# Optimization experiments

Measured on AMD Instinct MI355X. Metric: run time of the kernel, lower is better.

The kernel has to match this reference:

```python
import jax, jax.numpy as jnp
import numpy as np

N_NODES = 50000
N_EDGES = 400000
N_GRAPHS = 512
F = 32        # num_features
NB = 32       # mp_num_basis_fn
ZMAX = 118
CUTOFF = 5.0
NSPH = 9      # (mp_max_degree+1)^2 with max_degree=2
DEG_IDX = jnp.array([0, 1, 1, 1, 2, 2, 2, 2, 2])  # degree of each spherical component


def _bernstein(u, n=NB):
    # reciprocal_bernstein radial basis: Bernstein polynomials of degree n-1 at u in [0,1)
    k = jnp.arange(n, dtype=jnp.float32)
    log_binom = (jax.scipy.special.gammaln(float(n)) - jax.scipy.special.gammaln(k + 1.0)
                 - jax.scipy.special.gammaln(float(n) - k))
    u = jnp.clip(u, 1e-7, 1.0 - 1e-7)[..., None]
    return jnp.exp(log_binom + k * jnp.log(u) + (float(n) - 1.0 - k) * jnp.log1p(-u))


def _smooth_cutoff(r, cutoff=CUTOFF):
    t = r / cutoff
    return jnp.where(t < 1.0, jnp.exp(1.0 - 1.0 / jnp.clip(1.0 - t * t, 1e-7, None)), 0.0)


def _sph(u):
    # real spherical harmonics (cartesian normalization) up to degree 2; u: (E,3) unit vectors
    x, y, z = u[:, 0], u[:, 1], u[:, 2]
    c = jnp.sqrt(jnp.float32(3.0))
    return jnp.stack([jnp.ones_like(x), y, z, x,
                      c * x * y, c * y * z, 0.5 * (3.0 * z * z - 1.0),
                      c * z * x, 0.5 * c * (x * x - y * y)], axis=-1)


def _dense(x, W, b):
    # equivariant Dense: shared kernel over spherical components, bias only on scalar (l=0)
    y = jnp.einsum('nmf,fg->nmg', x, W)
    return y.at[:, 0, :].add(b)


def _silu_gate(x):
    # equivariant silu: scalar channel gates all degrees (scalar part -> exact silu)
    return x * jax.nn.sigmoid(x[:, 0:1, :])


def setup_inputs() -> dict:
    key = jax.random.key(0)
    ks = jax.random.split(key, 24)
    s = 1.0 / np.sqrt(F)
    sb = 1.0 / np.sqrt(NB)
    inp = {
        'positions': 2.0 * jax.random.normal(ks[0], (N_NODES, 3), jnp.float32),
        'embed': jax.random.normal(ks[1], (ZMAX, F), jnp.float32),
        'Wy0': sb * jax.random.normal(ks[2], (3, NB, F), jnp.float32),
        'Wx0': sb * jax.random.normal(ks[3], (3, NB, F), jnp.float32),
        'W1_0': s * jax.random.normal(ks[4], (F, F), jnp.float32),
        'b1_0': jnp.zeros((F,), jnp.float32),
        'W2_0': s * jax.random.normal(ks[5], (F, F), jnp.float32),
        'b2_0': jnp.zeros((F,), jnp.float32),
        'c0': jnp.full((1,), 0.5, jnp.float32),
        'Wr_last': sb * jax.random.normal(ks[6], (NB, F), jnp.float32),
        'W1_1': s * jax.random.normal(ks[7], (F, F), jnp.float32),
        'b1_1': jnp.zeros((F,), jnp.float32),
        'W2_1': s * jax.random.normal(ks[8], (F, F), jnp.float32),
        'b2_1': jnp.zeros((F,), jnp.float32),
        'c1': jnp.full((1,), 0.5, jnp.float32),
        'Wro1': s * jax.random.normal(ks[9], (F, F), jnp.float32),
        'bro1': jnp.zeros((F,), jnp.float32),
        'Wro2': s * jax.random.normal(ks[10], (F, 1), jnp.float32),
        'bro2': jnp.zeros((1,), jnp.float32),
        'atomic_bias': jax.random.normal(ks[11], (ZMAX,), jnp.float32),
        'atomic_numbers': jax.random.randint(ks[12], (N_NODES,), 0, ZMAX, jnp.int32),
        'dst_idx': jax.random.randint(ks[13], (N_EDGES,), 0, N_NODES, jnp.int32),
        'src_idx': jax.random.randint(ks[14], (N_EDGES,), 0, N_NODES, jnp.int32),
        'batch_segments': jnp.sort(jax.random.randint(ks[15], (N_NODES,), 0, N_GRAPHS, jnp.int32)),
        'graph_mask': jnp.ones((N_GRAPHS,), jnp.bool_),
    }
    return inp


def reference(positions, embed, Wy0, Wx0, W1_0, b1_0, W2_0, b2_0, c0,
              Wr_last, W1_1, b1_1, W2_1, b2_1, c1,
              Wro1, bro1, Wro2, bro2, atomic_bias,
              atomic_numbers, dst_idx, src_idx, batch_segments, graph_mask):
    # --- edge geometry (gather_src/gather_dst) ---
    disp = positions[src_idx] - positions[dst_idx]                # (E,3)
    r = jnp.sqrt(jnp.sum(disp * disp, axis=-1) + 1e-12)           # (E,)
    u = disp / r[:, None]
    Y = _sph(u)                                                   # (E,9)
    rbf = _bernstein(r / (r + 1.0)) * _smooth_cutoff(r)[:, None]  # (E,NB)

    # --- atomic embedding, lifted to (N, 9, F) with zero higher degrees ---
    x0 = embed[atomic_numbers]                                    # (N,F)
    x = jnp.concatenate([x0[:, None, :], jnp.zeros((N_NODES, NSPH - 1, F), x0.dtype)], axis=1)

    # --- iteration 0: full-degree equivariant message pass ---
    wy = jnp.einsum('eb,lbf->elf', rbf, Wy0)[:, DEG_IDX, :]       # (E,9,F) radial weights, (0,l)->l path
    wx = jnp.einsum('eb,lbf->elf', rbf, Wx0)[:, DEG_IDX, :]       # (l,0)->l path
    xs = x[src_idx]                                               # (E,9,F)
    msg = wy * Y[:, :, None] * xs[:, 0:1, :] + wx * xs
    y = jax.ops.segment_sum(msg, dst_idx, num_segments=N_NODES)   # (N,9,F)
    y = x + y
    y = _silu_gate(_dense(y, W1_0, b1_0))
    y = _dense(y, W2_0, b2_0)
    x = x + jax.nn.silu(c0) * y                                   # y_nl == 0 (era disabled)

    # --- iteration 1 (last): max_degree=0 message pass, then reduce to scalars ---
    w0 = rbf @ Wr_last                                            # (E,F)
    msg0 = w0 * x[src_idx, 0, :]
    y0 = jax.ops.segment_sum(msg0, dst_idx, num_segments=N_NODES) # (N,F)
    xs0 = x[:, 0, :]                                              # change_max_degree -> scalars
    y0 = xs0 + y0
    y0 = jax.nn.silu(y0 @ W1_1 + b1_1)
    y0 = y0 @ W2_1 + b2_1
    xs0 = xs0 + jax.nn.silu(c1) * y0

    # --- atomic readout and per-graph sum ---
    h = jax.nn.silu(xs0 @ Wro1 + bro1)
    e_atom = (h @ Wro2)[:, 0] + bro2[0] + atomic_bias[atomic_numbers]
    e_graph = jax.ops.segment_sum(e_atom, batch_segments, num_segments=N_GRAPHS)
    return jnp.where(graph_mask, e_graph, 0.0)
```

## Files before the change

### kernel.cpp

```cpp
#include <hip/hip_runtime.h>
#include <math.h>

#define NNODES 50000
#define NEDGES 400000
#define NGRAPHS 512
#define FDIM 32
#define CAP 32

#define NHALVES 4096
#define NQ   (NNODES / NHALVES)
#define NREM (NNODES % NHALVES)

static constexpr float BINOM31[32] = {
    1.f, 31.f, 465.f, 4495.f, 31465.f, 169911.f, 736281.f, 2629575.f,
    7888725.f, 20160075.f, 44352165.f, 84672315.f, 141120525.f, 206253075.f,
    265182525.f, 300540195.f, 300540195.f, 265182525.f, 206253075.f,
    141120525.f, 84672315.f, 44352165.f, 20160075.f, 7888725.f, 2629575.f,
    736281.f, 169911.f, 31465.f, 4495.f, 465.f, 31.f, 1.f
};

__device__ __forceinline__ float fast_rcp(float x) {
    return __builtin_amdgcn_rcpf(x);
}
__device__ __forceinline__ float silu(float x) {
    return x * fast_rcp(1.0f + __expf(-x));
}

__global__ __launch_bounds__(256) void build_csr(
    const float* __restrict__ pos,
    const int* __restrict__ srci, const int* __restrict__ dsti,
    const int* __restrict__ Z,
    float4* __restrict__ pay, int* __restrict__ deg)
{
    int e = blockIdx.x * 256 + threadIdx.x;
    if (e >= NEDGES) return;
    int s = srci[e], d = dsti[e];
    float dx = pos[3 * s]     - pos[3 * d];
    float dy = pos[3 * s + 1] - pos[3 * d + 1];
    float dz = pos[3 * s + 2] - pos[3 * d + 2];
    float r = sqrtf(dx * dx + dy * dy + dz * dz + 1e-12f);
    if (r >= 5.0f) return;

    float t = r * 0.2f;
    float q = fmaxf(1.0f - t * t, 1e-7f);
    float cut = __expf(1.0f - fast_rcp(q));
    float v = fast_rcp(r + 1.0f);
    float v2 = v * v, v4 = v2 * v2, v8 = v4 * v4, v16 = v8 * v8;
    float scale = v16 * v8 * v4 * v2 * v * cut;

    int rank = atomicAdd(&deg[d], 1);
    if (rank < CAP)
        pay[(size_t)d * CAP + rank] =
            make_float4(r, scale,
                        __int_as_float(s * FDIM),
                        __int_as_float(Z[s] * FDIM));
}

#define GATHER8(ACC, XSRC, SEL)                                            \
    float ACC = 0.0f;                                                      \
    for (int j = 0; j < dgc; j += 8) {                                     \
        float rr[8], sc[8], xg[8], hh[8];                                  \
        _Pragma("unroll")                                                  \
        for (int k = 0; k < 8; ++k) {                                      \
            float4 _p = pl[j + k];                                         \
            rr[k] = _p.x; sc[k] = _p.y;                                    \
            xg[k] = (XSRC)[__float_as_int(_p.SEL) + f];                    \
        }                                                                  \
        _Pragma("unroll")                                                  \
        for (int k = 0; k < 8; ++k) hh[k] = cw[31];                        \
        _Pragma("unroll")                                                  \
        for (int t = 30; t >= 0; --t) {                                    \
            _Pragma("unroll")                                              \
            for (int k = 0; k < 8; ++k)                                    \
                hh[k] = fmaf(hh[k], rr[k], cw[t]);                         \
        }                                                                  \
        _Pragma("unroll")                                                  \
        for (int k = 0; k < 8; ++k)                                        \
            ACC = fmaf(sc[k] * hh[k], xg[k], ACC);                         \
    }

#define MATVEC32R(RES, WR, BIAS) do {                                      \
    float4 _q0=yp[0], _q1=yp[1], _q2=yp[2], _q3=yp[3];                     \
    float4 _q4=yp[4], _q5=yp[5], _q6=yp[6], _q7=yp[7];                     \
    float _a0=(BIAS), _a1=0.f, _a2=0.f, _a3=0.f;                           \
    _a0=fmaf(_q0.x,WR[ 0],_a0); _a0=fmaf(_q0.y,WR[ 1],_a0);                \
    _a0=fmaf(_q0.z,WR[ 2],_a0); _a0=fmaf(_q0.w,WR[ 3],_a0);                \
    _a1=fmaf(_q1.x,WR[ 4],_a1); _a1=fmaf(_q1.y,WR[ 5],_a1);                \
    _a1=fmaf(_q1.z,WR[ 6],_a1); _a1=fmaf(_q1.w,WR[ 7],_a1);                \
    _a2=fmaf(_q2.x,WR[ 8],_a2); _a2=fmaf(_q2.y,WR[ 9],_a2);                \
    _a2=fmaf(_q2.z,WR[10],_a2); _a2=fmaf(_q2.w,WR[11],_a2);                \
    _a3=fmaf(_q3.x,WR[12],_a3); _a3=fmaf(_q3.y,WR[13],_a3);                \
    _a3=fmaf(_q3.z,WR[14],_a3); _a3=fmaf(_q3.w,WR[15],_a3);                \
    _a0=fmaf(_q4.x,WR[16],_a0); _a0=fmaf(_q4.y,WR[17],_a0);                \
    _a0=fmaf(_q4.z,WR[18],_a0); _a0=fmaf(_q4.w,WR[19],_a0);                \
    _a1=fmaf(_q5.x,WR[20],_a1); _a1=fmaf(_q5.y,WR[21],_a1);                \
    _a1=fmaf(_q5.z,WR[22],_a1); _a1=fmaf(_q5.w,WR[23],_a1);                \
    _a2=fmaf(_q6.x,WR[24],_a2); _a2=fmaf(_q6.y,WR[25],_a2);                \
    _a2=fmaf(_q6.z,WR[26],_a2); _a2=fmaf(_q6.w,WR[27],_a2);                \
    _a3=fmaf(_q7.x,WR[28],_a3); _a3=fmaf(_q7.y,WR[29],_a3);                \
    _a3=fmaf(_q7.z,WR[30],_a3); _a3=fmaf(_q7.w,WR[31],_a3);                \
    RES = (_a0+_a1)+(_a2+_a3); } while (0)

__device__ __forceinline__ void half_range(int h, int& n0, int& n1) {
    int a = h < NREM ? h * (NQ + 1) : NREM * (NQ + 1) + (h - NREM) * NQ;
    n0 = a;
    n1 = a + (h < NREM ? NQ + 1 : NQ);
}

__global__ __launch_bounds__(256, 2) void fused_a(
    const float4* __restrict__ pay, const int* __restrict__ deg,
    const float* __restrict__ embed, const int* __restrict__ Z,
    const float* __restrict__ Wy0, const float* __restrict__ Wx0,
    const float* __restrict__ W1, const float* __restrict__ b1,
    const float* __restrict__ W2, const float* __restrict__ b2,
    const float* __restrict__ c0,
    float* __restrict__ x1buf)
{
    __shared__ __align__(16) float ylds[4][64];
    __shared__ __align__(16) float4 plds[4][2][CAP];
    int tid = threadIdx.x;
    int widx = tid >> 6;
    int lane = tid & 63;
    int f    = lane & 31;
    int half = lane >> 5;

    float cw[32], w1r[32], w2r[32];
    #pragma unroll
    for (int k = 0; k < 32; ++k) {
        cw[k]  = BINOM31[k] * (Wy0[k * FDIM + f] + Wx0[k * FDIM + f]);
        w1r[k] = W1[k * FDIM + f];
        w2r[k] = W2[k * FDIM + f];
    }
    float b1f = b1[f], b2f = b2[f];
    float sc0 = silu(c0[0]);

    int hidx = (blockIdx.x * 4 + widx) * 2 + half;
    int n0, n1;
    half_range(hidx, n0, n1);

    float* yrow = &ylds[widx][half * 32];
    const float4* yp = (const float4*)yrow;
    float4* pl = &plds[widx][half][0];

    float4 pv0 = pay[(size_t)n0 * CAP + f];
    int dgc = min(deg[n0], CAP);
    int zc  = Z[n0];
    pl[f] = pv0;
    float x0 = embed[zc * FDIM + f];

    for (int n = n0; n < n1; ++n) {
        int nn = (n + 1 < n1) ? n + 1 : n;
        float4 pvn = pay[(size_t)nn * CAP + f];
        int dgn = min(deg[nn], CAP);
        int zn  = Z[nn];

        GATHER8(accv, embed, w)

        float x0n = embed[zn * FDIM + f];
        pl[f] = pvn;

        yrow[f] = x0 + accv;
        float t;
        MATVEC32R(t, w1r, b1f);
        t = silu(t);
        yrow[f] = t;
        float u;
        MATVEC32R(u, w2r, b2f);
        x1buf[(size_t)n * FDIM + f] = fmaf(sc0, u, x0);

        dgc = dgn; x0 = x0n; zc = zn;
    }
}

__global__ __launch_bounds__(256, 2) void fused_b(
    const float4* __restrict__ pay, const int* __restrict__ deg,
    const float* __restrict__ x1buf, const float* __restrict__ Wr_last,
    const float* __restrict__ W1, const float* __restrict__ b1,
    const float* __restrict__ W2, const float* __restrict__ b2,
    const float* __restrict__ c1,
    const float* __restrict__ Wro1, const float* __restrict__ bro1,
    const float* __restrict__ Wro2, const float* __restrict__ bro2,
    const float* __restrict__ abias, const int* __restrict__ Z,
    const int* __restrict__ segs,
    float* __restrict__ out)
{
    __shared__ __align__(16) float ylds[4][64];
    __shared__ __align__(16) float4 plds[4][2][CAP];
    int tid = threadIdx.x;
    int widx = tid >> 6;
    int lane = tid & 63;
    int f    = lane & 31;
    int half = lane >> 5;

    float cw[32], w1r[32], w2r[32], wrr[32];
    #pragma unroll
    for (int k = 0; k < 32; ++k) {
        cw[k]  = BINOM31[k] * Wr_last[k * FDIM + f];
        w1r[k] = W1[k * FDIM + f];
        w2r[k] = W2[k * FDIM + f];
        wrr[k] = Wro1[k * FDIM + f];
    }
    float b1f = b1[f], b2f = b2[f], bro1f = bro1[f], wro2f = Wro2[f];
    float sc1 = silu(c1[0]);
    float bro2v = bro2[0];

    int hidx = (blockIdx.x * 4 + widx) * 2 + half;
    int n0, n1;
    half_range(hidx, n0, n1);

    float* yrow = &ylds[widx][half * 32];
    const float4* yp = (const float4*)yrow;
    float4* pl = &plds[widx][half][0];

    float4 pv0 = pay[(size_t)n0 * CAP + f];
    int dgc = min(deg[n0], CAP);
    int zc  = Z[n0];
    int sg  = segs[n0];
    pl[f] = pv0;
    float x1 = x1buf[(size_t)n0 * FDIM + f];
    float ab = abias[zc];

    float segacc = 0.0f;
    int   curseg = -1;

    for (int n = n0; n < n1; ++n) {
        int nn = (n + 1 < n1) ? n + 1 : n;
        float4 pvn = pay[(size_t)nn * CAP + f];
        int dgn = min(deg[nn], CAP);
        int zn  = Z[nn];
        int sgn = segs[nn];

        GATHER8(accv, x1buf, z)

        float x1n = x1buf[(size_t)nn * FDIM + f];
        float abn = abias[zn];
        pl[f] = pvn;

        yrow[f] = x1 + accv;
        float t;
        MATVEC32R(t, w1r, b1f);
        t = silu(t);
        yrow[f] = t;
        float u;
        MATVEC32R(u, w2r, b2f);
        float xs0 = fmaf(sc1, u, x1);
        yrow[f] = xs0;
        float h;
        MATVEC32R(h, wrr, bro1f);
        float p = silu(h) * wro2f;
        p += __shfl_xor(p, 16, 32);
        p += __shfl_xor(p, 8, 32);
        p += __shfl_xor(p, 4, 32);
        p += __shfl_xor(p, 2, 32);
        p += __shfl_xor(p, 1, 32);

        if (f == 0) {
            float e = p + bro2v + ab;
            if (sg == curseg) segacc += e;
            else {
                if (curseg >= 0) atomicAdd(&out[curseg], segacc);
                curseg = sg; segacc = e;
            }
        }

        dgc = dgn; x1 = x1n; ab = abn; sg = sgn; zc = zn;
    }
    if (f == 0 && curseg >= 0) atomicAdd(&out[curseg], segacc);
}

extern "C" void kernel_launch(void* const* d_in, const int* in_sizes, int n_in,
                              void* d_out, int out_size, void* d_ws, size_t ws_size,
                              hipStream_t stream)
{
    const float* pos     = (const float*)d_in[0];
    const float* embed   = (const float*)d_in[1];
    const float* Wy0     = (const float*)d_in[2];
    const float* Wx0     = (const float*)d_in[3];
    const float* W1_0    = (const float*)d_in[4];
    const float* b1_0    = (const float*)d_in[5];
    const float* W2_0    = (const float*)d_in[6];
    const float* b2_0    = (const float*)d_in[7];
    const float* c0      = (const float*)d_in[8];
    const float* Wr_last = (const float*)d_in[9];
    const float* W1_1    = (const float*)d_in[10];
    const float* b1_1    = (const float*)d_in[11];
    const float* W2_1    = (const float*)d_in[12];
    const float* b2_1    = (const float*)d_in[13];
    const float* c1      = (const float*)d_in[14];
    const float* Wro1    = (const float*)d_in[15];
    const float* bro1    = (const float*)d_in[16];
    const float* Wro2    = (const float*)d_in[17];
    const float* bro2    = (const float*)d_in[18];
    const float* abias   = (const float*)d_in[19];
    const int*   Z       = (const int*)d_in[20];
    const int*   dsti    = (const int*)d_in[21];
    const int*   srci    = (const int*)d_in[22];
    const int*   segs    = (const int*)d_in[23];

    float* out = (float*)d_out;

    char* w = (char*)d_ws;
    float4* pay   = (float4*)w;  w += (size_t)NNODES * CAP * 16;
    float*  x1buf = (float*)w;   w += (size_t)NNODES * FDIM * 4;
    int*    deg   = (int*)w;     w += (size_t)NNODES * 4;

    const int edgeBlocks = (NEDGES + 255) / 256;
    const int persBlocks = NHALVES / 8;

    hipMemsetAsync(pay, 0, (size_t)NNODES * CAP * 16, stream);
    hipMemsetAsync(deg, 0, (size_t)NNODES * 4, stream);
    hipMemsetAsync(out, 0, (size_t)NGRAPHS * 4, stream);

    build_csr<<<edgeBlocks, 256, 0, stream>>>(pos, srci, dsti, Z, pay, deg);
    fused_a<<<persBlocks, 256, 0, stream>>>(pay, deg, embed, Z, Wy0, Wx0,
                                            W1_0, b1_0, W2_0, b2_0, c0, x1buf);
    fused_b<<<persBlocks, 256, 0, stream>>>(pay, deg, x1buf, Wr_last,
                                            W1_1, b1_1, W2_1, b2_1, c1,
                                            Wro1, bro1, Wro2, bro2,
                                            abias, Z, segs, out);
}
```

Before: 185.0 us.

## Move matvec weights to swizzled LDS, raise occupancy, drop payload memset

Second and readout weight matrices move from per-thread registers into XOR-swizzled shared memory columns read as float4, which frees registers so launch bounds can target 4 blocks per CU. The number of persistent work halves doubles to give more waves. The 25MB payload memset is removed and payload loads are masked by degree, so stale slots are never read. In exchange, matvecs now read LDS instead of registers, and each block does extra setup work plus a barrier before its main loop.

```diff
diff --git a/kernel.cpp b/kernel.cpp
--- a/kernel.cpp
+++ b/kernel.cpp
@@ -7,7 +7,7 @@
 #define FDIM 32
 #define CAP 32
 
-#define NHALVES 4096
+#define NHALVES 8192
 #define NQ   (NNODES / NHALVES)
 #define NREM (NNODES % NHALVES)
 
@@ -54,6 +54,10 @@
             make_float4(r, scale,
                         __int_as_float(s * FDIM),
                         __int_as_float(Z[s] * FDIM));
+}
+
+__device__ __forceinline__ int wcol_idx(int k, int f) {
+    return f * 64 + ((((k >> 2) ^ (f & 15))) << 2) + (k & 3);
 }
 
 #define GATHER8(ACC, XSRC, SEL)                                            \
@@ -101,13 +105,31 @@
     _a3=fmaf(_q7.z,WR[30],_a3); _a3=fmaf(_q7.w,WR[31],_a3);                \
     RES = (_a0+_a1)+(_a2+_a3); } while (0)
 
+#define MATVEC32C(RES, WC, BIAS) do {                                      \
+    const float4* _w4 = (const float4*)(WC);                               \
+    float _a0=(BIAS), _a1=0.f, _a2=0.f, _a3=0.f;                           \
+    _Pragma("unroll")                                                      \
+    for (int c = 0; c < 8; ++c) {                                          \
+        float4 _wc = _w4[(f << 4) + (c ^ (f & 15))];                       \
+        float4 _qc = yp[c];                                                \
+        float _s = fmaf(_qc.x, _wc.x, 0.f);                                \
+        _s = fmaf(_qc.y, _wc.y, _s);                                       \
+        _s = fmaf(_qc.z, _wc.z, _s);                                       \
+        _s = fmaf(_qc.w, _wc.w, _s);                                       \
+        if ((c & 3) == 0) _a0 += _s;                                       \
+        else if ((c & 3) == 1) _a1 += _s;                                  \
+        else if ((c & 3) == 2) _a2 += _s;                                  \
+        else _a3 += _s;                                                    \
+    }                                                                      \
+    RES = (_a0+_a1)+(_a2+_a3); } while (0)
+
 __device__ __forceinline__ void half_range(int h, int& n0, int& n1) {
     int a = h < NREM ? h * (NQ + 1) : NREM * (NQ + 1) + (h - NREM) * NQ;
     n0 = a;
     n1 = a + (h < NREM ? NQ + 1 : NQ);
 }
 
-__global__ __launch_bounds__(256, 2) void fused_a(
+__global__ __launch_bounds__(256, 4) void fused_a(
     const float4* __restrict__ pay, const int* __restrict__ deg,
     const float* __restrict__ embed, const int* __restrict__ Z,
     const float* __restrict__ Wy0, const float* __restrict__ Wx0,
@@ -118,21 +140,26 @@
 {
     __shared__ __align__(16) float ylds[4][64];
     __shared__ __align__(16) float4 plds[4][2][CAP];
+    __shared__ __align__(16) float w2c[FDIM * 64];
     int tid = threadIdx.x;
     int widx = tid >> 6;
     int lane = tid & 63;
     int f    = lane & 31;
     int half = lane >> 5;
 
-    float cw[32], w1r[32], w2r[32];
+    float cw[32], w1r[32];
     #pragma unroll
     for (int k = 0; k < 32; ++k) {
         cw[k]  = BINOM31[k] * (Wy0[k * FDIM + f] + Wx0[k * FDIM + f]);
         w1r[k] = W1[k * FDIM + f];
-        w2r[k] = W2[k * FDIM + f];
+    }
+    for (int i = tid; i < FDIM * FDIM; i += 256) {
+        int k = i >> 5, ff = i & 31;
+        w2c[wcol_idx(k, ff)] = W2[i];
     }
     float b1f = b1[f], b2f = b2[f];
     float sc0 = silu(c0[0]);
+    __syncthreads();
 
     int hidx = (blockIdx.x * 4 + widx) * 2 + half;
     int n0, n1;
@@ -142,17 +169,19 @@
     const float4* yp = (const float4*)yrow;
     float4* pl = &plds[widx][half][0];
 
-    float4 pv0 = pay[(size_t)n0 * CAP + f];
     int dgc = min(deg[n0], CAP);
-    int zc  = Z[n0];
+    float4 pv0 = make_float4(0.f, 0.f, 0.f, 0.f);
+    if (f < dgc) pv0 = pay[(size_t)n0 * CAP + f];
+    int zc = Z[n0];
     pl[f] = pv0;
     float x0 = embed[zc * FDIM + f];
 
     for (int n = n0; n < n1; ++n) {
         int nn = (n + 1 < n1) ? n + 1 : n;
-        float4 pvn = pay[(size_t)nn * CAP + f];
         int dgn = min(deg[nn], CAP);
         int zn  = Z[nn];
+        float4 pvn = make_float4(0.f, 0.f, 0.f, 0.f);
+        if (f < dgn) pvn = pay[(size_t)nn * CAP + f];
 
         GATHER8(accv, embed, w)
 
@@ -165,14 +194,14 @@
         t = silu(t);
         yrow[f] = t;
         float u;
-        MATVEC32R(u, w2r, b2f);
+        MATVEC32C(u, w2c, b2f);
         x1buf[(size_t)n * FDIM + f] = fmaf(sc0, u, x0);
 
         dgc = dgn; x0 = x0n; zc = zn;
     }
 }
 
-__global__ __launch_bounds__(256, 2) void fused_b(
+__global__ __launch_bounds__(256, 4) void fused_b(
     const float4* __restrict__ pay, const int* __restrict__ deg,
     const float* __restrict__ x1buf, const float* __restrict__ Wr_last,
     const float* __restrict__ W1, const float* __restrict__ b1,
@@ -186,23 +215,29 @@
 {
     __shared__ __align__(16) float ylds[4][64];
     __shared__ __align__(16) float4 plds[4][2][CAP];
+    __shared__ __align__(16) float w2c[FDIM * 64];
+    __shared__ __align__(16) float wrc[FDIM * 64];
     int tid = threadIdx.x;
     int widx = tid >> 6;
     int lane = tid & 63;
     int f    = lane & 31;
     int half = lane >> 5;
 
-    float cw[32], w1r[32], w2r[32], wrr[32];
+    float cw[32], w1r[32];
     #pragma unroll
     for (int k = 0; k < 32; ++k) {
         cw[k]  = BINOM31[k] * Wr_last[k * FDIM + f];
         w1r[k] = W1[k * FDIM + f];
-        w2r[k] = W2[k * FDIM + f];
-        wrr[k] = Wro1[k * FDIM + f];
+    }
+    for (int i = tid; i < FDIM * FDIM; i += 256) {
+        int k = i >> 5, ff = i & 31;
+        w2c[wcol_idx(k, ff)] = W2[i];
+        wrc[wcol_idx(k, ff)] = Wro1[i];
     }
     float b1f = b1[f], b2f = b2[f], bro1f = bro1[f], wro2f = Wro2[f];
     float sc1 = silu(c1[0]);
     float bro2v = bro2[0];
+    __syncthreads();
 
     int hidx = (blockIdx.x * 4 + widx) * 2 + half;
     int n0, n1;
@@ -212,10 +247,11 @@
     const float4* yp = (const float4*)yrow;
     float4* pl = &plds[widx][half][0];
 
-    float4 pv0 = pay[(size_t)n0 * CAP + f];
     int dgc = min(deg[n0], CAP);
-    int zc  = Z[n0];
-    int sg  = segs[n0];
+    float4 pv0 = make_float4(0.f, 0.f, 0.f, 0.f);
+    if (f < dgc) pv0 = pay[(size_t)n0 * CAP + f];
+    int zc = Z[n0];
+    int sg = segs[n0];
     pl[f] = pv0;
     float x1 = x1buf[(size_t)n0 * FDIM + f];
     float ab = abias[zc];
@@ -225,10 +261,11 @@
 
     for (int n = n0; n < n1; ++n) {
         int nn = (n + 1 < n1) ? n + 1 : n;
-        float4 pvn = pay[(size_t)nn * CAP + f];
         int dgn = min(deg[nn], CAP);
         int zn  = Z[nn];
         int sgn = segs[nn];
+        float4 pvn = make_float4(0.f, 0.f, 0.f, 0.f);
+        if (f < dgn) pvn = pay[(size_t)nn * CAP + f];
 
         GATHER8(accv, x1buf, z)
 
@@ -242,11 +279,11 @@
         t = silu(t);
         yrow[f] = t;
         float u;
-        MATVEC32R(u, w2r, b2f);
+        MATVEC32C(u, w2c, b2f);
         float xs0 = fmaf(sc1, u, x1);
         yrow[f] = xs0;
         float h;
-        MATVEC32R(h, wrr, bro1f);
+        MATVEC32C(h, wrc, bro1f);
         float p = silu(h) * wro2f;
         p += __shfl_xor(p, 16, 32);
         p += __shfl_xor(p, 8, 32);
@@ -307,7 +344,6 @@
     const int edgeBlocks = (NEDGES + 255) / 256;
     const int persBlocks = NHALVES / 8;
 
-    hipMemsetAsync(pay, 0, (size_t)NNODES * CAP * 16, stream);
     hipMemsetAsync(deg, 0, (size_t)NNODES * 4, stream);
     hipMemsetAsync(out, 0, (size_t)NGRAPHS * 4, stream);
 
```

Result: slower. 305.3 us (+65.0%).
